# Kernel optimization log

Hardware: AMD Instinct MI355X
Metric: run time of the kernel (lower is better)

Reference implementation:

```python
import jax, jax.numpy as jnp
import numpy as np


def setup_inputs() -> dict:
    key = jax.random.key(0)
    k1, k2, k3, k4, k5 = jax.random.split(key, 5)
    B, S, H, F, E = 2, 512, 1024, 3584, 8
    scale_in = 1.0 / np.sqrt(H)
    scale_ff = 1.0 / np.sqrt(F)
    return {
        "hidden_states": jax.random.normal(k1, (B, S, H), dtype=jnp.float32),
        "gate_w": jax.random.normal(k2, (E, H), dtype=jnp.float32) * scale_in,
        "w1": jax.random.normal(k3, (E, F, H), dtype=jnp.float32) * scale_in,
        "w2": jax.random.normal(k4, (E, H, F), dtype=jnp.float32) * scale_ff,
        "w3": jax.random.normal(k5, (E, F, H), dtype=jnp.float32) * scale_in,
    }


TOP_K = 2


def reference(hidden_states, gate_w, w1, w2, w3):
    B, S, H = hidden_states.shape
    E = gate_w.shape[0]
    x = hidden_states.reshape(B * S, H)  # [T, H]
    T = x.shape[0]

    # Router: softmax in fp32, top-2 selection, renormalize selected weights.
    router_logits = x @ gate_w.T  # [T, E]
    probs = jax.nn.softmax(router_logits.astype(jnp.float32), axis=-1)
    top_vals, top_idx = jax.lax.top_k(probs, TOP_K)  # [T, K]
    top_vals = top_vals / jnp.sum(top_vals, axis=-1, keepdims=True)
    top_vals = top_vals.astype(x.dtype)

    # Dense routing-weight matrix [T, E]: weight if selected else 0
    # (equivalent to the one-hot expert_mask + index_add combine).
    dense_w = jnp.zeros((T, E), dtype=x.dtype).at[
        jnp.arange(T)[:, None], top_idx
    ].add(top_vals)

    # Expert SwiGLU MLPs, batched over the expert axis.
    h1 = jnp.einsum("th,efh->etf", x, w1)  # [E, T, F]
    h3 = jnp.einsum("th,efh->etf", x, w3)  # [E, T, F]
    y = jnp.einsum("etf,ehf->eth", jax.nn.silu(h1) * h3, w2)  # [E, T, H]

    # Weighted combine across experts.
    out = jnp.einsum("eth,te->th", y, dense_w)  # [T, H]
    return out.reshape(B, S, H), router_logits
```

## Files before the change

### kernel.cpp

```cpp
#include <hip/hip_runtime.h>
#include <hip/hip_bf16.h>

typedef __bf16 v8bf __attribute__((ext_vector_type(8)));
typedef __bf16 v4bf __attribute__((ext_vector_type(4)));
typedef float  f32x4 __attribute__((ext_vector_type(4)));

#define NTOK 1024
#define HDIM 1024
#define FDIM 3584
#define NEXP 8
#define NPAIR 2048
#define MAXTILES 24

#define OFF_COUNTS   0
#define OFF_OFFSETS  64
#define OFF_NTILES   128
#define OFF_TILE_E   192
#define OFF_TILE_M   320
#define OFF_TOKIDX   1024
#define OFF_TOKWT    (1024 + 4*NPAIR)
#define OFF_PAIRTOK  (OFF_TOKWT + 4*NPAIR)
#define OFF_PAIRWT   (OFF_PAIRTOK + 4*NPAIR)
#define OFF_SLOTOF   (OFF_PAIRWT + 4*NPAIR)
#define OFF_ACT      65536
#define OFF_Y        (OFF_ACT + 2ull*NPAIR*FDIM)

static __device__ inline v4bf cvt4(float4 f) {
    v4bf r;
    r[0] = (__bf16)f.x; r[1] = (__bf16)f.y; r[2] = (__bf16)f.z; r[3] = (__bf16)f.w;
    return r;
}

#define BAR() do { asm volatile("s_waitcnt lgkmcnt(0)" ::: "memory"); \
                   __builtin_amdgcn_s_barrier(); } while (0)

__global__ __launch_bounds__(256) void moe_router(
    const float* __restrict__ x, const float* __restrict__ gw,
    float* __restrict__ logits, int* __restrict__ counts,
    int* __restrict__ tok_idx, float* __restrict__ tok_wt)
{
    const int lane = threadIdx.x & 63;
    const int wv = threadIdx.x >> 6;
    const int t = blockIdx.x * 4 + wv;
    const float* xr = x + (size_t)t * HDIM;

    float acc[NEXP];
#pragma unroll
    for (int e = 0; e < NEXP; ++e) acc[e] = 0.f;
#pragma unroll
    for (int j = 0; j < 4; ++j) {
        int h = lane * 4 + j * 256;
        float4 xv = *(const float4*)(xr + h);
#pragma unroll
        for (int e = 0; e < NEXP; ++e) {
            float4 g = *(const float4*)(gw + e * HDIM + h);
            acc[e] += xv.x * g.x + xv.y * g.y + xv.z * g.z + xv.w * g.w;
        }
    }
#pragma unroll
    for (int e = 0; e < NEXP; ++e) {
#pragma unroll
        for (int s = 32; s > 0; s >>= 1) acc[e] += __shfl_xor(acc[e], s);
    }
    if (lane == 0) {
#pragma unroll
        for (int e = 0; e < NEXP; ++e) logits[t * NEXP + e] = acc[e];
        int i0 = 0;
#pragma unroll
        for (int e = 1; e < NEXP; ++e) if (acc[e] > acc[i0]) i0 = e;
        int i1 = (i0 == 0) ? 1 : 0;
#pragma unroll
        for (int e = 0; e < NEXP; ++e) if (e != i0 && acc[e] > acc[i1]) i1 = e;
        float w0 = 1.f / (1.f + expf(acc[i1] - acc[i0]));
        float w1 = 1.f - w0;
        tok_idx[2 * t] = i0; tok_idx[2 * t + 1] = i1;
        tok_wt[2 * t] = w0;  tok_wt[2 * t + 1] = w1;
        atomicAdd(&counts[i0], 1);
        atomicAdd(&counts[i1], 1);
    }
}

__global__ void moe_scatter(const int* __restrict__ counts, const int* __restrict__ tok_idx,
                            const float* __restrict__ tok_wt, int* __restrict__ offsets,
                            int* __restrict__ pair_token, float* __restrict__ pair_wt,
                            int* __restrict__ slot_of, int* __restrict__ tile_e,
                            int* __restrict__ tile_m, int* __restrict__ ntiles)
{
    __shared__ int cur[NEXP];
    const int tid = threadIdx.x;
    if (tid == 0) {
        int run = 0, nt = 0;
        for (int e = 0; e < NEXP; ++e) {
            offsets[e] = run; cur[e] = run;
            for (int m0 = 0; m0 < counts[e]; m0 += 128) {
                tile_e[nt] = e; tile_m[nt] = m0; ++nt;
            }
            run += counts[e];
        }
        *ntiles = nt;
    }
    __syncthreads();
    for (int p = tid; p < 2 * NTOK; p += blockDim.x) {
        int e = tok_idx[p];
        int s = atomicAdd(&cur[e], 1);
        pair_token[s] = p >> 1;
        pair_wt[s] = tok_wt[p];
        slot_of[p] = s;
    }
}

__global__ __launch_bounds__(256, 2) void moe_gemm1(
    const float* __restrict__ x, const float* __restrict__ w1g,
    const float* __restrict__ w3g, const int* __restrict__ counts,
    const int* __restrict__ offsets, const int* __restrict__ pair_token,
    const int* __restrict__ tile_e, const int* __restrict__ tile_m,
    const int* __restrict__ ntiles,
    __bf16* __restrict__ act)
{
    const int ty = blockIdx.y;
    if (ty >= *ntiles) return;
    const int e = tile_e[ty];
    const int m0 = tile_m[ty];
    const int Me = counts[e];
    const int rows = min(128, Me - m0);
    const int slot0 = offsets[e] + m0;
    const int n0 = blockIdx.x * 128;

    __shared__ __align__(16) __bf16 As[2][128 * 32];
    __shared__ __align__(16) __bf16 B1s[2][128 * 32];
    __shared__ __align__(16) __bf16 B3s[2][128 * 32];

    const int tid = threadIdx.x;
    const int lane = tid & 63;
    const int wv = tid >> 6;
    const int wm = (wv >> 1) * 64;
    const int wn = (wv & 1) * 64;
    const int lr = lane & 15;
    const int lk = (lane >> 4) * 8;

    f32x4 acc1[4][4], acc3[4][4];
#pragma unroll
    for (int i = 0; i < 4; ++i)
#pragma unroll
        for (int j = 0; j < 4; ++j) {
            acc1[i][j] = (f32x4){0.f, 0.f, 0.f, 0.f};
            acc3[i][j] = (f32x4){0.f, 0.f, 0.f, 0.f};
        }

    const ptrdiff_t d31 = w3g - w1g;
    const float* aptr[4];
    const float* b1p[4];
    int wof[4];
#pragma unroll
    for (int i = 0; i < 4; ++i) {
        int flat = tid + i * 256;
        int r = flat >> 3;
        int c = (flat & 7) * 4;
        int rr = (r < rows) ? r : 0;
        aptr[i] = x + (size_t)pair_token[slot0 + rr] * HDIM + c;
        b1p[i]  = w1g + ((size_t)e * FDIM + n0 + r) * HDIM + c;
        wof[i]  = r * 32 + c;
    }

    float4 av[4], b1v[4], b3v[4];
#define LOADK1(K0) do { _Pragma("unroll") \
    for (int i = 0; i < 4; ++i) { \
        av[i]  = *(const float4*)(aptr[i] + (K0)); \
        b1v[i] = *(const float4*)(b1p[i] + (K0)); \
        b3v[i] = *(const float4*)(b1p[i] + d31 + (K0)); \
    } } while (0)

    LOADK1(0);
    int cur = 0;
    for (int k0 = 0; k0 < HDIM; k0 += 32) {
#pragma unroll
        for (int i = 0; i < 4; ++i) {
            *(v4bf*)&As[cur][wof[i]]  = cvt4(av[i]);
            *(v4bf*)&B1s[cur][wof[i]] = cvt4(b1v[i]);
            *(v4bf*)&B3s[cur][wof[i]] = cvt4(b3v[i]);
        }
        if (k0 + 32 < HDIM) LOADK1(k0 + 32);
        BAR();
        v8bf af[4], b1f[4], b3f[4];
#pragma unroll
        for (int i = 0; i < 4; ++i) {
            af[i]  = *(const v8bf*)&As[cur][(wm + i * 16 + lr) * 32 + lk];
            b1f[i] = *(const v8bf*)&B1s[cur][(wn + i * 16 + lr) * 32 + lk];
            b3f[i] = *(const v8bf*)&B3s[cur][(wn + i * 16 + lr) * 32 + lk];
        }
#pragma unroll
        for (int mi = 0; mi < 4; ++mi)
#pragma unroll
            for (int ni = 0; ni < 4; ++ni) {
                acc1[mi][ni] = __builtin_amdgcn_mfma_f32_16x16x32_bf16(af[mi], b1f[ni], acc1[mi][ni], 0, 0, 0);
                acc3[mi][ni] = __builtin_amdgcn_mfma_f32_16x16x32_bf16(af[mi], b3f[ni], acc3[mi][ni], 0, 0, 0);
            }
        cur ^= 1;
    }

    const int rj = (lane >> 4) * 4;
#pragma unroll
    for (int mi = 0; mi < 4; ++mi) {
#pragma unroll
        for (int j = 0; j < 4; ++j) {
            int rm = wm + mi * 16 + rj + j;
            if (rm < rows) {
                size_t rowoff = (size_t)(slot0 + rm) * FDIM + n0 + wn;
#pragma unroll
                for (int ni = 0; ni < 4; ++ni) {
                    float h1 = acc1[mi][ni][j];
                    float h3 = acc3[mi][ni][j];
                    float sv = (h1 / (1.f + __expf(-h1))) * h3;
                    act[rowoff + ni * 16 + lr] = (__bf16)sv;
                }
            }
        }
    }
}

__global__ __launch_bounds__(256, 2) void moe_gemm2(
    const __bf16* __restrict__ act, const float* __restrict__ w2g,
    const int* __restrict__ counts, const int* __restrict__ offsets,
    const int* __restrict__ tile_e, const int* __restrict__ tile_m,
    const int* __restrict__ ntiles,
    float* __restrict__ y)
{
    const int ty = blockIdx.y;
    if (ty >= *ntiles) return;
    const int e = tile_e[ty];
    const int m0 = tile_m[ty];
    const int Me = counts[e];
    const int rows = min(128, Me - m0);
    const int slot0 = offsets[e] + m0;
    const int n0 = blockIdx.x * 64;

    __shared__ __align__(16) __bf16 As[2][128 * 32];
    __shared__ __align__(16) __bf16 Bs[2][64 * 32];

    const int tid = threadIdx.x;
    const int lane = tid & 63;
    const int wv = tid >> 6;
    const int wm = (wv >> 1) * 64;
    const int wn = (wv & 1) * 32;
    const int lr = lane & 15;
    const int lk = (lane >> 4) * 8;

    f32x4 acc[4][2];
#pragma unroll
    for (int i = 0; i < 4; ++i)
#pragma unroll
        for (int j = 0; j < 2; ++j) acc[i][j] = (f32x4){0.f, 0.f, 0.f, 0.f};

    const __bf16* ap[2];
    int awof[2];
#pragma unroll
    for (int i = 0; i < 2; ++i) {
        int flat = tid + i * 256;
        int r = flat >> 2;
        int c = (flat & 3) * 8;
        int rr = (r < rows) ? r : 0;
        ap[i]   = act + (size_t)(slot0 + rr) * FDIM + c;
        awof[i] = r * 32 + c;
    }
    const float* bp[2];
    int bwof[2];
#pragma unroll
    for (int i = 0; i < 2; ++i) {
        int flat = tid + i * 256;
        int r = flat >> 3;
        int c = (flat & 7) * 4;
        bp[i]   = w2g + ((size_t)e * HDIM + n0 + r) * FDIM + c;
        bwof[i] = r * 32 + c;
    }

    v8bf a8[2];
    float4 bv[2];
#define LOADK2(K0) do { _Pragma("unroll") \
    for (int i = 0; i < 2; ++i) { \
        a8[i] = *(const v8bf*)(ap[i] + (K0)); \
        bv[i] = *(const float4*)(bp[i] + (K0)); \
    } } while (0)

    LOADK2(0);
    int cur = 0;
    for (int k0 = 0; k0 < FDIM; k0 += 32) {
#pragma unroll
        for (int i = 0; i < 2; ++i) {
            *(v8bf*)&As[cur][awof[i]] = a8[i];
            *(v4bf*)&Bs[cur][bwof[i]] = cvt4(bv[i]);
        }
        if (k0 + 32 < FDIM) LOADK2(k0 + 32);
        BAR();
        v8bf af[4], bf[2];
#pragma unroll
        for (int i = 0; i < 4; ++i)
            af[i] = *(const v8bf*)&As[cur][(wm + i * 16 + lr) * 32 + lk];
#pragma unroll
        for (int i = 0; i < 2; ++i)
            bf[i] = *(const v8bf*)&Bs[cur][(wn + i * 16 + lr) * 32 + lk];
#pragma unroll
        for (int mi = 0; mi < 4; ++mi)
#pragma unroll
            for (int ni = 0; ni < 2; ++ni)
                acc[mi][ni] = __builtin_amdgcn_mfma_f32_16x16x32_bf16(af[mi], bf[ni], acc[mi][ni], 0, 0, 0);
        cur ^= 1;
    }

    const int rj = (lane >> 4) * 4;
#pragma unroll
    for (int mi = 0; mi < 4; ++mi) {
#pragma unroll
        for (int j = 0; j < 4; ++j) {
            int rm = wm + mi * 16 + rj + j;
            if (rm < rows) {
                size_t rowoff = (size_t)(slot0 + rm) * HDIM + n0 + wn;
#pragma unroll
                for (int ni = 0; ni < 2; ++ni)
                    y[rowoff + ni * 16 + lr] = acc[mi][ni][j];
            }
        }
    }
}

__global__ __launch_bounds__(256) void moe_combine(
    const float* __restrict__ y, const int* __restrict__ slot_of,
    const float* __restrict__ pair_wt, float* __restrict__ out)
{
    const int t = blockIdx.x;
    const int tid = threadIdx.x;
    const int s0 = slot_of[2 * t];
    const int s1 = slot_of[2 * t + 1];
    const float w0 = pair_wt[s0];
    const float w1 = pair_wt[s1];
    const float4 a = *(const float4*)(y + (size_t)s0 * HDIM + tid * 4);
    const float4 b = *(const float4*)(y + (size_t)s1 * HDIM + tid * 4);
    float4 o;
    o.x = w0 * a.x + w1 * b.x;
    o.y = w0 * a.y + w1 * b.y;
    o.z = w0 * a.z + w1 * b.z;
    o.w = w0 * a.w + w1 * b.w;
    *(float4*)(out + (size_t)t * HDIM + tid * 4) = o;
}

extern "C" void kernel_launch(void* const* d_in, const int* in_sizes, int n_in,
                              void* d_out, int out_size, void* d_ws, size_t ws_size,
                              hipStream_t stream) {
    const float* x   = (const float*)d_in[0];
    const float* gw  = (const float*)d_in[1];
    const float* w1  = (const float*)d_in[2];
    const float* w2  = (const float*)d_in[3];
    const float* w3  = (const float*)d_in[4];

    float* out    = (float*)d_out;
    float* logits = out + (size_t)NTOK * HDIM;

    char* ws = (char*)d_ws;
    int*    counts     = (int*)(ws + OFF_COUNTS);
    int*    offsets    = (int*)(ws + OFF_OFFSETS);
    int*    ntiles     = (int*)(ws + OFF_NTILES);
    int*    tile_e     = (int*)(ws + OFF_TILE_E);
    int*    tile_m     = (int*)(ws + OFF_TILE_M);
    int*    tok_idx    = (int*)(ws + OFF_TOKIDX);
    float*  tok_wt     = (float*)(ws + OFF_TOKWT);
    int*    pair_token = (int*)(ws + OFF_PAIRTOK);
    float*  pair_wt    = (float*)(ws + OFF_PAIRWT);
    int*    slot_of    = (int*)(ws + OFF_SLOTOF);
    __bf16* act        = (__bf16*)(ws + OFF_ACT);
    float*  yb         = (float*)(ws + OFF_Y);

    hipMemsetAsync(counts, 0, 64, stream);

    moe_router<<<dim3(NTOK / 4), dim3(256), 0, stream>>>(x, gw, logits, counts, tok_idx, tok_wt);
    moe_scatter<<<dim3(1), dim3(256), 0, stream>>>(counts, tok_idx, tok_wt, offsets,
                                                   pair_token, pair_wt, slot_of,
                                                   tile_e, tile_m, ntiles);
    moe_gemm1<<<dim3(FDIM / 128, MAXTILES), dim3(256), 0, stream>>>(
        x, w1, w3, counts, offsets, pair_token, tile_e, tile_m, ntiles, act);
    moe_gemm2<<<dim3(HDIM / 64, MAXTILES), dim3(256), 0, stream>>>(
        act, w2, counts, offsets, tile_e, tile_m, ntiles, yb);
    moe_combine<<<dim3(NTOK), dim3(256), 0, stream>>>(yb, slot_of, pair_wt, out);
}
```

Baseline: 234.6 us.

## Shrink GEMM tiles for more blocks, separate gemm2 tile list, unroll double buffer

The first GEMM's N tile is halved from 128 to 64. The second GEMM now uses 64-row M tiles from its own tile list, which the scatter kernel builds, and is launched with a higher occupancy bound. Both main loops are unrolled by two over explicit ping-pong shared buffers with separate register prefetch sets. The aim is to raise the number of blocks across the many compute units and to improve latency hiding. The cost is less data reuse per tile and more redundant weight and activation loads.

```diff
diff --git a/kernel.cpp b/kernel.cpp
--- a/kernel.cpp
+++ b/kernel.cpp
@@ -10,13 +10,17 @@
 #define FDIM 3584
 #define NEXP 8
 #define NPAIR 2048
-#define MAXTILES 24
+#define MAXT1 24
+#define MAXT2 40
 
 #define OFF_COUNTS   0
 #define OFF_OFFSETS  64
-#define OFF_NTILES   128
-#define OFF_TILE_E   192
-#define OFF_TILE_M   320
+#define OFF_NT1      128
+#define OFF_NT2      132
+#define OFF_T1E      192
+#define OFF_T1M      320
+#define OFF_T2E      448
+#define OFF_T2M      640
 #define OFF_TOKIDX   1024
 #define OFF_TOKWT    (1024 + 4*NPAIR)
 #define OFF_PAIRTOK  (OFF_TOKWT + 4*NPAIR)
@@ -83,21 +87,21 @@
 __global__ void moe_scatter(const int* __restrict__ counts, const int* __restrict__ tok_idx,
                             const float* __restrict__ tok_wt, int* __restrict__ offsets,
                             int* __restrict__ pair_token, float* __restrict__ pair_wt,
-                            int* __restrict__ slot_of, int* __restrict__ tile_e,
-                            int* __restrict__ tile_m, int* __restrict__ ntiles)
+                            int* __restrict__ slot_of,
+                            int* __restrict__ t1e, int* __restrict__ t1m, int* __restrict__ nt1,
+                            int* __restrict__ t2e, int* __restrict__ t2m, int* __restrict__ nt2)
 {
     __shared__ int cur[NEXP];
     const int tid = threadIdx.x;
     if (tid == 0) {
-        int run = 0, nt = 0;
+        int run = 0, n1 = 0, n2 = 0;
         for (int e = 0; e < NEXP; ++e) {
             offsets[e] = run; cur[e] = run;
-            for (int m0 = 0; m0 < counts[e]; m0 += 128) {
-                tile_e[nt] = e; tile_m[nt] = m0; ++nt;
-            }
+            for (int m0 = 0; m0 < counts[e]; m0 += 128) { t1e[n1] = e; t1m[n1] = m0; ++n1; }
+            for (int m0 = 0; m0 < counts[e]; m0 += 64)  { t2e[n2] = e; t2m[n2] = m0; ++n2; }
             run += counts[e];
         }
-        *ntiles = nt;
+        *nt1 = n1; *nt2 = n2;
     }
     __syncthreads();
     for (int p = tid; p < 2 * NTOK; p += blockDim.x) {
@@ -113,90 +117,104 @@
     const float* __restrict__ x, const float* __restrict__ w1g,
     const float* __restrict__ w3g, const int* __restrict__ counts,
     const int* __restrict__ offsets, const int* __restrict__ pair_token,
-    const int* __restrict__ tile_e, const int* __restrict__ tile_m,
-    const int* __restrict__ ntiles,
+    const int* __restrict__ t1e, const int* __restrict__ t1m,
+    const int* __restrict__ nt1,
     __bf16* __restrict__ act)
 {
     const int ty = blockIdx.y;
-    if (ty >= *ntiles) return;
-    const int e = tile_e[ty];
-    const int m0 = tile_m[ty];
+    if (ty >= *nt1) return;
+    const int e = t1e[ty];
+    const int m0 = t1m[ty];
     const int Me = counts[e];
     const int rows = min(128, Me - m0);
     const int slot0 = offsets[e] + m0;
-    const int n0 = blockIdx.x * 128;
+    const int n0 = blockIdx.x * 64;
 
     __shared__ __align__(16) __bf16 As[2][128 * 32];
-    __shared__ __align__(16) __bf16 B1s[2][128 * 32];
-    __shared__ __align__(16) __bf16 B3s[2][128 * 32];
+    __shared__ __align__(16) __bf16 B1s[2][64 * 32];
+    __shared__ __align__(16) __bf16 B3s[2][64 * 32];
 
     const int tid = threadIdx.x;
     const int lane = tid & 63;
     const int wv = tid >> 6;
     const int wm = (wv >> 1) * 64;
-    const int wn = (wv & 1) * 64;
+    const int wn = (wv & 1) * 32;
     const int lr = lane & 15;
     const int lk = (lane >> 4) * 8;
 
-    f32x4 acc1[4][4], acc3[4][4];
+    f32x4 acc1[4][2], acc3[4][2];
 #pragma unroll
     for (int i = 0; i < 4; ++i)
 #pragma unroll
-        for (int j = 0; j < 4; ++j) {
+        for (int j = 0; j < 2; ++j) {
             acc1[i][j] = (f32x4){0.f, 0.f, 0.f, 0.f};
             acc3[i][j] = (f32x4){0.f, 0.f, 0.f, 0.f};
         }
 
     const ptrdiff_t d31 = w3g - w1g;
     const float* aptr[4];
-    const float* b1p[4];
-    int wof[4];
+    int awof[4];
 #pragma unroll
     for (int i = 0; i < 4; ++i) {
-        int flat = tid + i * 256;
-        int r = flat >> 3;
-        int c = (flat & 7) * 4;
+        int slot = tid + i * 256;
+        int r = slot >> 3;
+        int c = (slot & 7) * 4;
         int rr = (r < rows) ? r : 0;
         aptr[i] = x + (size_t)pair_token[slot0 + rr] * HDIM + c;
-        b1p[i]  = w1g + ((size_t)e * FDIM + n0 + r) * HDIM + c;
-        wof[i]  = r * 32 + c;
-    }
-
-    float4 av[4], b1v[4], b3v[4];
-#define LOADK1(K0) do { _Pragma("unroll") \
-    for (int i = 0; i < 4; ++i) { \
-        av[i]  = *(const float4*)(aptr[i] + (K0)); \
-        b1v[i] = *(const float4*)(b1p[i] + (K0)); \
-        b3v[i] = *(const float4*)(b1p[i] + d31 + (K0)); \
-    } } while (0)
-
-    LOADK1(0);
-    int cur = 0;
-    for (int k0 = 0; k0 < HDIM; k0 += 32) {
-#pragma unroll
-        for (int i = 0; i < 4; ++i) {
-            *(v4bf*)&As[cur][wof[i]]  = cvt4(av[i]);
-            *(v4bf*)&B1s[cur][wof[i]] = cvt4(b1v[i]);
-            *(v4bf*)&B3s[cur][wof[i]] = cvt4(b3v[i]);
-        }
-        if (k0 + 32 < HDIM) LOADK1(k0 + 32);
+        awof[i] = r * 32 + c;
+    }
+    const float* bp[2];
+    int bwof[2];
+#pragma unroll
+    for (int i = 0; i < 2; ++i) {
+        int slot = tid + i * 256;
+        int r = slot >> 3;
+        int c = (slot & 7) * 4;
+        bp[i]   = w1g + ((size_t)e * FDIM + n0 + r) * HDIM + c;
+        bwof[i] = r * 32 + c;
+    }
+
+    float4 a0[4], b10[2], b30[2];
+    float4 a1[4], b11[2], b31[2];
+
+#define LD1(AV, B1V, B3V, K0) do { _Pragma("unroll") \
+    for (int i = 0; i < 4; ++i) AV[i] = *(const float4*)(aptr[i] + (K0)); \
+    _Pragma("unroll") \
+    for (int i = 0; i < 2; ++i) { B1V[i] = *(const float4*)(bp[i] + (K0)); \
+                                  B3V[i] = *(const float4*)(bp[i] + d31 + (K0)); } } while (0)
+
+#define ST1(BUF, AV, B1V, B3V) do { _Pragma("unroll") \
+    for (int i = 0; i < 4; ++i) *(v4bf*)&As[BUF][awof[i]] = cvt4(AV[i]); \
+    _Pragma("unroll") \
+    for (int i = 0; i < 2; ++i) { *(v4bf*)&B1s[BUF][bwof[i]] = cvt4(B1V[i]); \
+                                  *(v4bf*)&B3s[BUF][bwof[i]] = cvt4(B3V[i]); } } while (0)
+
+#define CMP1(BUF) do { v8bf af[4], b1f[2], b3f[2]; _Pragma("unroll") \
+    for (int i = 0; i < 4; ++i) af[i] = *(const v8bf*)&As[BUF][(wm + i * 16 + lr) * 32 + lk]; \
+    _Pragma("unroll") \
+    for (int i = 0; i < 2; ++i) { b1f[i] = *(const v8bf*)&B1s[BUF][(wn + i * 16 + lr) * 32 + lk]; \
+                                  b3f[i] = *(const v8bf*)&B3s[BUF][(wn + i * 16 + lr) * 32 + lk]; } \
+    _Pragma("unroll") \
+    for (int mi = 0; mi < 4; ++mi) { _Pragma("unroll") \
+        for (int ni = 0; ni < 2; ++ni) { \
+            acc1[mi][ni] = __builtin_amdgcn_mfma_f32_16x16x32_bf16(af[mi], b1f[ni], acc1[mi][ni], 0, 0, 0); \
+            acc3[mi][ni] = __builtin_amdgcn_mfma_f32_16x16x32_bf16(af[mi], b3f[ni], acc3[mi][ni], 0, 0, 0); } } } while (0)
+
+    LD1(a0, b10, b30, 0);
+    LD1(a1, b11, b31, 32);
+    for (int k0 = 0; k0 < HDIM; k0 += 64) {
+        ST1(0, a0, b10, b30);
+        if (k0 + 64 < HDIM) LD1(a0, b10, b30, k0 + 64);
         BAR();
-        v8bf af[4], b1f[4], b3f[4];
-#pragma unroll
-        for (int i = 0; i < 4; ++i) {
-            af[i]  = *(const v8bf*)&As[cur][(wm + i * 16 + lr) * 32 + lk];
-            b1f[i] = *(const v8bf*)&B1s[cur][(wn + i * 16 + lr) * 32 + lk];
-            b3f[i] = *(const v8bf*)&B3s[cur][(wn + i * 16 + lr) * 32 + lk];
-        }
-#pragma unroll
-        for (int mi = 0; mi < 4; ++mi)
-#pragma unroll
-            for (int ni = 0; ni < 4; ++ni) {
-                acc1[mi][ni] = __builtin_amdgcn_mfma_f32_16x16x32_bf16(af[mi], b1f[ni], acc1[mi][ni], 0, 0, 0);
-                acc3[mi][ni] = __builtin_amdgcn_mfma_f32_16x16x32_bf16(af[mi], b3f[ni], acc3[mi][ni], 0, 0, 0);
-            }
-        cur ^= 1;
-    }
+        CMP1(0);
+        ST1(1, a1, b11, b31);
+        if (k0 + 96 < HDIM) LD1(a1, b11, b31, k0 + 96);
+        BAR();
+        CMP1(1);
+    }
+#undef LD1
+#undef ST1
+#undef CMP1
 
     const int rj = (lane >> 4) * 4;
 #pragma unroll
@@ -207,7 +225,7 @@
             if (rm < rows) {
                 size_t rowoff = (size_t)(slot0 + rm) * FDIM + n0 + wn;
 #pragma unroll
-                for (int ni = 0; ni < 4; ++ni) {
+                for (int ni = 0; ni < 2; ++ni) {
                     float h1 = acc1[mi][ni][j];
                     float h3 = acc3[mi][ni][j];
                     float sv = (h1 / (1.f + __expf(-h1))) * h3;
@@ -218,97 +236,95 @@
     }
 }
 
-__global__ __launch_bounds__(256, 2) void moe_gemm2(
+__global__ __launch_bounds__(256, 4) void moe_gemm2(
     const __bf16* __restrict__ act, const float* __restrict__ w2g,
     const int* __restrict__ counts, const int* __restrict__ offsets,
-    const int* __restrict__ tile_e, const int* __restrict__ tile_m,
-    const int* __restrict__ ntiles,
+    const int* __restrict__ t2e, const int* __restrict__ t2m,
+    const int* __restrict__ nt2,
     float* __restrict__ y)
 {
     const int ty = blockIdx.y;
-    if (ty >= *ntiles) return;
-    const int e = tile_e[ty];
-    const int m0 = tile_m[ty];
+    if (ty >= *nt2) return;
+    const int e = t2e[ty];
+    const int m0 = t2m[ty];
     const int Me = counts[e];
-    const int rows = min(128, Me - m0);
+    const int rows = min(64, Me - m0);
     const int slot0 = offsets[e] + m0;
     const int n0 = blockIdx.x * 64;
 
-    __shared__ __align__(16) __bf16 As[2][128 * 32];
+    __shared__ __align__(16) __bf16 As[2][64 * 32];
     __shared__ __align__(16) __bf16 Bs[2][64 * 32];
 
     const int tid = threadIdx.x;
     const int lane = tid & 63;
     const int wv = tid >> 6;
-    const int wm = (wv >> 1) * 64;
+    const int wm = (wv >> 1) * 32;
     const int wn = (wv & 1) * 32;
     const int lr = lane & 15;
     const int lk = (lane >> 4) * 8;
 
-    f32x4 acc[4][2];
-#pragma unroll
-    for (int i = 0; i < 4; ++i)
+    f32x4 acc[2][2];
+#pragma unroll
+    for (int i = 0; i < 2; ++i)
 #pragma unroll
         for (int j = 0; j < 2; ++j) acc[i][j] = (f32x4){0.f, 0.f, 0.f, 0.f};
 
-    const __bf16* ap[2];
-    int awof[2];
-#pragma unroll
-    for (int i = 0; i < 2; ++i) {
-        int flat = tid + i * 256;
-        int r = flat >> 2;
-        int c = (flat & 3) * 8;
+    const __bf16* ap;
+    int awof;
+    {
+        int r = tid >> 2;
+        int c = (tid & 3) * 8;
         int rr = (r < rows) ? r : 0;
-        ap[i]   = act + (size_t)(slot0 + rr) * FDIM + c;
-        awof[i] = r * 32 + c;
+        ap   = act + (size_t)(slot0 + rr) * FDIM + c;
+        awof = r * 32 + c;
     }
     const float* bp[2];
     int bwof[2];
 #pragma unroll
     for (int i = 0; i < 2; ++i) {
-        int flat = tid + i * 256;
-        int r = flat >> 3;
-        int c = (flat & 7) * 4;
+        int slot = tid + i * 256;
+        int r = slot >> 3;
+        int c = (slot & 7) * 4;
         bp[i]   = w2g + ((size_t)e * HDIM + n0 + r) * FDIM + c;
         bwof[i] = r * 32 + c;
     }
 
-    v8bf a8[2];
-    float4 bv[2];
-#define LOADK2(K0) do { _Pragma("unroll") \
-    for (int i = 0; i < 2; ++i) { \
-        a8[i] = *(const v8bf*)(ap[i] + (K0)); \
-        bv[i] = *(const float4*)(bp[i] + (K0)); \
-    } } while (0)
-
-    LOADK2(0);
-    int cur = 0;
-    for (int k0 = 0; k0 < FDIM; k0 += 32) {
-#pragma unroll
-        for (int i = 0; i < 2; ++i) {
-            *(v8bf*)&As[cur][awof[i]] = a8[i];
-            *(v4bf*)&Bs[cur][bwof[i]] = cvt4(bv[i]);
-        }
-        if (k0 + 32 < FDIM) LOADK2(k0 + 32);
+    v8bf a8_0, a8_1;
+    float4 bv0[2], bv1[2];
+
+#define LD2(A8, BV, K0) do { A8 = *(const v8bf*)(ap + (K0)); _Pragma("unroll") \
+    for (int i = 0; i < 2; ++i) BV[i] = *(const float4*)(bp[i] + (K0)); } while (0)
+
+#define ST2(BUF, A8, BV) do { *(v8bf*)&As[BUF][awof] = A8; _Pragma("unroll") \
+    for (int i = 0; i < 2; ++i) *(v4bf*)&Bs[BUF][bwof[i]] = cvt4(BV[i]); } while (0)
+
+#define CMP2(BUF) do { v8bf af[2], bf[2]; _Pragma("unroll") \
+    for (int i = 0; i < 2; ++i) { af[i] = *(const v8bf*)&As[BUF][(wm + i * 16 + lr) * 32 + lk]; \
+                                  bf[i] = *(const v8bf*)&Bs[BUF][(wn + i * 16 + lr) * 32 + lk]; } \
+    _Pragma("unroll") \
+    for (int mi = 0; mi < 2; ++mi) { _Pragma("unroll") \
+        for (int ni = 0; ni < 2; ++ni) \
+            acc[mi][ni] = __builtin_amdgcn_mfma_f32_16x16x32_bf16(af[mi], bf[ni], acc[mi][ni], 0, 0, 0); } } while (0)
+
+    LD2(a8_0, bv0, 0);
+    LD2(a8_1, bv1, 32);
+    for (int k0 = 0; k0 < FDIM; k0 += 64) {
+        ST2(0, a8_0, bv0);
+        if (k0 + 64 < FDIM) LD2(a8_0, bv0, k0 + 64);
         BAR();
-        v8bf af[4], bf[2];
-#pragma unroll
-        for (int i = 0; i < 4; ++i)
-            af[i] = *(const v8bf*)&As[cur][(wm + i * 16 + lr) * 32 + lk];
-#pragma unroll
-        for (int i = 0; i < 2; ++i)
-            bf[i] = *(const v8bf*)&Bs[cur][(wn + i * 16 + lr) * 32 + lk];
-#pragma unroll
-        for (int mi = 0; mi < 4; ++mi)
-#pragma unroll
-            for (int ni = 0; ni < 2; ++ni)
-                acc[mi][ni] = __builtin_amdgcn_mfma_f32_16x16x32_bf16(af[mi], bf[ni], acc[mi][ni], 0, 0, 0);
-        cur ^= 1;
-    }
+        CMP2(0);
+        ST2(1, a8_1, bv1);
+        if (k0 + 96 < FDIM) LD2(a8_1, bv1, k0 + 96);
+        BAR();
+        CMP2(1);
+    }
+#undef LD2
+#undef ST2
+#undef CMP2
 
     const int rj = (lane >> 4) * 4;
 #pragma unroll
-    for (int mi = 0; mi < 4; ++mi) {
+    for (int mi = 0; mi < 2; ++mi) {
 #pragma unroll
         for (int j = 0; j < 4; ++j) {
             int rm = wm + mi * 16 + rj + j;
@@ -357,9 +373,12 @@
     char* ws = (char*)d_ws;
     int*    counts     = (int*)(ws + OFF_COUNTS);
     int*    offsets    = (int*)(ws + OFF_OFFSETS);
-    int*    ntiles     = (int*)(ws + OFF_NTILES);
-    int*    tile_e     = (int*)(ws + OFF_TILE_E);
-    int*    tile_m     = (int*)(ws + OFF_TILE_M);
+    int*    nt1        = (int*)(ws + OFF_NT1);
+    int*    nt2        = (int*)(ws + OFF_NT2);
+    int*    t1e        = (int*)(ws + OFF_T1E);
+    int*    t1m        = (int*)(ws + OFF_T1M);
+    int*    t2e        = (int*)(ws + OFF_T2E);
+    int*    t2m        = (int*)(ws + OFF_T2M);
     int*    tok_idx    = (int*)(ws + OFF_TOKIDX);
     float*  tok_wt     = (float*)(ws + OFF_TOKWT);
     int*    pair_token = (int*)(ws + OFF_PAIRTOK);
@@ -373,10 +392,10 @@
     moe_router<<<dim3(NTOK / 4), dim3(256), 0, stream>>>(x, gw, logits, counts, tok_idx, tok_wt);
     moe_scatter<<<dim3(1), dim3(256), 0, stream>>>(counts, tok_idx, tok_wt, offsets,
                                                    pair_token, pair_wt, slot_of,
-                                                   tile_e, tile_m, ntiles);
-    moe_gemm1<<<dim3(FDIM / 128, MAXTILES), dim3(256), 0, stream>>>(
-        x, w1, w3, counts, offsets, pair_token, tile_e, tile_m, ntiles, act);
-    moe_gemm2<<<dim3(HDIM / 64, MAXTILES), dim3(256), 0, stream>>>(
-        act, w2, counts, offsets, tile_e, tile_m, ntiles, yb);
+                                                   t1e, t1m, nt1, t2e, t2m, nt2);
+    moe_gemm1<<<dim3(FDIM / 64, MAXT1), dim3(256), 0, stream>>>(
+        x, w1, w3, counts, offsets, pair_token, t1e, t1m, nt1, act);
+    moe_gemm2<<<dim3(HDIM / 64, MAXT2), dim3(256), 0, stream>>>(
+        act, w2, counts, offsets, t2e, t2m, nt2, yb);
     moe_combine<<<dim3(NTOK), dim3(256), 0, stream>>>(yb, slot_of, pair_wt, out);
 }
```

Measured after the change: 210.4 us. 1.11x faster.
